# Performance work log

Hardware: AMD Instinct MI355X
Metric: run time of the kernel (lower is better)

## Reference

```python
import jax, jax.numpy as jnp
import numpy as np

T, NI, NK, F, H, O, E = 8, 20000, 50000, 128, 256, 128, 500000


def setup_inputs() -> dict:
    key = jax.random.key(0)
    ks = jax.random.split(key, 32)
    s = 0.05
    inp = {
        "x_inf": jax.random.normal(ks[0], (T, NI, F), jnp.float32),
        "x_item": jax.random.normal(ks[1], (T, NK, F), jnp.float32),
        "e1_src": jax.random.randint(ks[2], (T, E), 0, NI, jnp.int32),
        "e1_dst": jax.random.randint(ks[3], (T, E), 0, NK, jnp.int32),
        "e2_src": jax.random.randint(ks[4], (T, E), 0, NK, jnp.int32),
        "e2_dst": jax.random.randint(ks[5], (T, E), 0, NI, jnp.int32),
        "target_idx": 1234,
        # layer 1, edge type a: influencer -> item (dst = item)
        "W1a_l": s * jax.random.normal(ks[6], (H, F), jnp.float32),
        "b1a_l": jnp.zeros((H,), jnp.float32),
        "W1a_r": s * jax.random.normal(ks[7], (H, F), jnp.float32),
        # layer 1, edge type b: item -> influencer (dst = influencer)
        "W1b_l": s * jax.random.normal(ks[8], (H, F), jnp.float32),
        "b1b_l": jnp.zeros((H,), jnp.float32),
        "W1b_r": s * jax.random.normal(ks[9], (H, F), jnp.float32),
        # layer 2, edge type a (dst = item; output unused by the model head, grads are zero)
        "W2a_l": s * jax.random.normal(ks[10], (O, H), jnp.float32),
        "b2a_l": jnp.zeros((O,), jnp.float32),
        "W2a_r": s * jax.random.normal(ks[11], (O, H), jnp.float32),
        # layer 2, edge type b (dst = influencer)
        "W2b_l": s * jax.random.normal(ks[12], (O, H), jnp.float32),
        "b2b_l": jnp.zeros((O,), jnp.float32),
        "W2b_r": s * jax.random.normal(ks[13], (O, H), jnp.float32),
        # GRU (PyTorch gate order: r, z, n)
        "W_ih": s * jax.random.normal(ks[14], (3 * H, O), jnp.float32),
        "W_hh": s * jax.random.normal(ks[15], (3 * H, H), jnp.float32),
        "b_ih": jnp.zeros((3 * H,), jnp.float32),
        "b_hh": jnp.zeros((3 * H,), jnp.float32),
        # attention + prediction head
        "W_att": s * jax.random.normal(ks[16], (1, H), jnp.float32),
        "b_att": jnp.zeros((1,), jnp.float32),
        "W_p1": s * jax.random.normal(ks[17], (H // 2, H), jnp.float32),
        "b_p1": jnp.zeros((H // 2,), jnp.float32),
        "W_p2": s * jax.random.normal(ks[18], (1, H // 2), jnp.float32),
        "b_p2": jnp.zeros((1,), jnp.float32),
    }
    return inp


def _sage(x_src, x_dst, src, dst, Wl, bl, Wr, n_dst):
    # PyG SAGEConv: lin_l(mean_j x_j) + lin_r(x_i); lin_l has bias, lin_r does not
    msg = x_src[src]                                            # [E, F]
    agg = jax.ops.segment_sum(msg, dst, num_segments=n_dst)     # [n_dst, F]
    cnt = jax.ops.segment_sum(jnp.ones_like(dst, dtype=x_src.dtype), dst, num_segments=n_dst)
    mean = agg / jnp.maximum(cnt, 1.0)[:, None]
    return mean @ Wl.T + bl + x_dst @ Wr.T


def reference(x_inf, x_item, e1_src, e1_dst, e2_src, e2_dst, target_idx,
              W1a_l, b1a_l, W1a_r, W1b_l, b1b_l, W1b_r,
              W2a_l, b2a_l, W2a_r, W2b_l, b2b_l, W2b_r,
              W_ih, W_hh, b_ih, b_hh, W_att, b_att, W_p1, b_p1, W_p2, b_p2):
    def step(carry, xs):
        xi, xk, s1, d1, s2, d2 = xs
        # hetero conv1 (aggr='sum' over edge types; each dst type has one incoming edge type)
        h_item = jax.nn.relu(_sage(xi, xk, s1, d1, W1a_l, b1a_l, W1a_r, NK))
        h_inf = jax.nn.relu(_sage(xk, xi, s2, d2, W1b_l, b1b_l, W1b_r, NI))
        # conv2: only the influencer output feeds the head (item output is dead code)
        o_inf = _sage(h_item, h_inf, s2, d2, W2b_l, b2b_l, W2b_r, NI)
        return carry, o_inf[target_idx]

    _, seq = jax.lax.scan(step, None, (x_inf, x_item, e1_src, e1_dst, e2_src, e2_dst))  # [T, O]

    def gru_step(h, x):
        gi = x @ W_ih.T + b_ih
        gh = h @ W_hh.T + b_hh
        i_r, i_z, i_n = jnp.split(gi, 3)
        h_r, h_z, h_n = jnp.split(gh, 3)
        r = jax.nn.sigmoid(i_r + h_r)
        z = jax.nn.sigmoid(i_z + h_z)
        n = jnp.tanh(i_n + r * h_n)
        h_new = (1.0 - z) * n + z * h
        return h_new, h_new

    h0 = jnp.zeros((H,), seq.dtype)
    _, rnn = jax.lax.scan(gru_step, h0, seq)                    # [T, H]

    att = jax.nn.softmax(rnn @ W_att.T + b_att, axis=0)         # [T, 1]
    ctx = jnp.sum(att * rnn, axis=0)                            # [H]
    hid = jax.nn.relu(ctx @ W_p1.T + b_p1)
    score = (hid @ W_p2.T + b_p2)[0]
    return score
```

## Files before the change

### kernel.cpp

```cpp
#include <hip/hip_runtime.h>
#include <math.h>

#define T 8
#define NI 20000
#define NK 50000
#define F 128
#define H 256
#define O 128
#define E 500000
#define G3 (3*H)
#define MAXS 256
#define CAP1 256
#define BMW 1568
#define NB 8
#define RPB 32
#define EQ (E/4)

#define OFF_CNT2   0
#define OFF_ITEMS  32
#define OFF_CNT1   (32 + T*MAXS*4)
#define OFF_HSUM   (OFF_CNT1 + T*MAXS*4)
#define OFF_BAR    (OFF_HSUM + T*H*4)
#define OFF_GBM    (OFF_BAR + 64)
#define WS_ZERO    (OFF_GBM + T*BMW*4)
#define OFF_LIST1  WS_ZERO
#define OFF_GI     (OFF_LIST1 + (size_t)T*MAXS*CAP1*4)
#define OFF_RNN    (OFF_GI + T*G3*4)
#define WS_USED    (OFF_RNN + T*H*4)

__global__ void k_find_e2(const int* __restrict__ e2_src, const int* __restrict__ e2_dst,
                          const int* __restrict__ target_p,
                          int* __restrict__ cnt2, int* __restrict__ items,
                          unsigned* __restrict__ gbm) {
    int t = blockIdx.y;
    long q = (long)blockIdx.x * 256 + threadIdx.x;
    if (q >= EQ) return;
    int target = *target_p;
    const int4 d4 = ((const int4*)(e2_dst + (long)t * E))[q];
    int dd[4] = {d4.x, d4.y, d4.z, d4.w};
#pragma unroll
    for (int c = 0; c < 4; ++c) {
        if (dd[c] == target) {
            long j = q * 4 + c;
            int src = e2_src[(long)t * E + j];
            int pos = atomicAdd(&cnt2[t], 1);
            if (pos < MAXS) {
                items[t * MAXS + pos] = src;
                atomicOr(&gbm[t * BMW + (src >> 5)], 1u << (src & 31));
            }
        }
    }
}

__global__ void k_scan_e1(const int* __restrict__ e1_src, const int* __restrict__ e1_dst,
                          const int* __restrict__ cnt2, const int* __restrict__ items,
                          const unsigned* __restrict__ gbm,
                          int* __restrict__ cnt1, int* __restrict__ list1) {
    int t = blockIdx.y;
    long q = (long)blockIdx.x * 256 + threadIdx.x;
    if (q >= EQ) return;
    const unsigned* bm = gbm + t * BMW;
    const int4 d4 = ((const int4*)(e1_dst + (long)t * E))[q];
    int dd[4] = {d4.x, d4.y, d4.z, d4.w};
#pragma unroll
    for (int c = 0; c < 4; ++c) {
        int d = dd[c];
        if (!((bm[d >> 5] >> (d & 31)) & 1u)) continue;
        long j = q * 4 + c;
        int src = e1_src[(long)t * E + j];
        int ns = min(cnt2[t], MAXS);
        for (int i = 0; i < ns; ++i) {
            if (items[t * MAXS + i] == d) {
                int pos = atomicAdd(&cnt1[t * MAXS + i], 1);
                if (pos < CAP1) list1[((long)t * MAXS + i) * CAP1 + pos] = src;
            }
        }
    }
}

__global__ void k_hitem(const float* __restrict__ x_item, const float* __restrict__ x_inf,
                        const float* __restrict__ W1a_l, const float* __restrict__ b1a_l,
                        const float* __restrict__ W1a_r,
                        const int* __restrict__ cnt2, const int* __restrict__ items,
                        const int* __restrict__ cnt1, const int* __restrict__ list1,
                        float* __restrict__ hsum) {
    int t = blockIdx.y, slot = blockIdx.x;
    int ns = min(cnt2[t], MAXS);
    if (slot >= ns) return;
    __shared__ float z1[F], xk[F];
    int item = items[t * MAXS + slot];
    int ne = cnt1[t * MAXS + slot];
    float inv = 1.0f / fmaxf((float)ne, 1.0f);
    int nr = min(ne, CAP1);
    if (threadIdx.x < F) {
        int f = threadIdx.x;
        const int* lst = list1 + ((long)t * MAXS + slot) * CAP1;
        float s = 0.0f;
        for (int e = 0; e < nr; ++e)
            s += x_inf[((long)t * NI + lst[e]) * F + f];
        z1[f] = s * inv;
        xk[f] = x_item[((long)t * NK + item) * F + f];
    }
    __syncthreads();
    int h = threadIdx.x;
    float acc = b1a_l[h];
    const float* wl = W1a_l + h * F;
    const float* wr = W1a_r + h * F;
    for (int f = 0; f < F; ++f) acc += z1[f] * wl[f] + xk[f] * wr[f];
    acc = fmaxf(acc, 0.0f);
    atomicAdd(&hsum[t * H + h], acc);
}

__global__ void __launch_bounds__(256, 1)
k_gru(const float* __restrict__ x_inf, const float* __restrict__ x_item,
      const int* __restrict__ target_p,
      const float* __restrict__ W1b_l, const float* __restrict__ b1b_l,
      const float* __restrict__ W1b_r,
      const float* __restrict__ W2b_l, const float* __restrict__ b2b_l,
      const float* __restrict__ W2b_r,
      const int* __restrict__ cnt2, const int* __restrict__ items,
      const float* __restrict__ hsum,
      const float* __restrict__ W_ih, const float* __restrict__ b_ih,
      const float* __restrict__ W_hh, const float* __restrict__ b_hh,
      const float* __restrict__ W_att, const float* __restrict__ b_att,
      const float* __restrict__ W_p1, const float* __restrict__ b_p1,
      const float* __restrict__ W_p2, const float* __restrict__ b_p2,
      float* __restrict__ gi, float* __restrict__ rnn,
      int* __restrict__ bar, float* __restrict__ out) {
    __shared__ float w[3 * RPB][H];
    __shared__ float h[H];
    __shared__ float srnn[T][H];
    __shared__ float satt[T], tmp[H], hid[128];
    __shared__ float z2[F], xt[F], hinf[H], mh[H], so[O];
    int b = blockIdx.x, tid = threadIdx.x;
    int wv = tid >> 6, lane = tid & 63;

    {
        int t = b;
        int target = *target_p;
        int ns = min(cnt2[t], MAXS);
        float c2 = fmaxf((float)cnt2[t], 1.0f);
        if (tid < F) {
            int f = tid;
            float s = 0.0f;
            for (int i = 0; i < ns; ++i)
                s += x_item[((long)t * NK + items[t * MAXS + i]) * F + f];
            z2[f] = s / c2;
            xt[f] = x_inf[((long)t * NI + target) * F + f];
        }
        __syncthreads();
        {
            float acc = b1b_l[tid];
            const float* wl = W1b_l + tid * F;
            const float* wr = W1b_r + tid * F;
            for (int f = 0; f < F; ++f) acc += z2[f] * wl[f] + xt[f] * wr[f];
            hinf[tid] = fmaxf(acc, 0.0f);
            mh[tid] = hsum[t * H + tid] / c2;
        }
        __syncthreads();
        if (tid < O) {
            float acc = b2b_l[tid];
            const float* wl = W2b_l + tid * H;
            const float* wr = W2b_r + tid * H;
            for (int k = 0; k < H; ++k) acc += mh[k] * wl[k] + hinf[k] * wr[k];
            so[tid] = acc;
        }
        __syncthreads();
        for (int row = wv; row < G3; row += 4) {
            const float* wih = W_ih + (long)row * O;
            float s = wih[lane] * so[lane] + wih[lane + 64] * so[lane + 64];
            for (int off = 32; off; off >>= 1) s += __shfl_down(s, off);
            if (lane == 0)
                __hip_atomic_store(&gi[t * G3 + row], s + b_ih[row],
                                   __ATOMIC_RELAXED, __HIP_MEMORY_SCOPE_AGENT);
        }
    }
    __syncthreads();
    if (tid == 0) {
        __threadfence();
        __hip_atomic_fetch_add(&bar[8], 1, __ATOMIC_RELEASE, __HIP_MEMORY_SCOPE_AGENT);
    }
    for (int idx = tid; idx < 3 * RPB * H; idx += 256) {
        int r = idx >> 8, k = idx & 255;
        int g = r / RPB, j = r - g * RPB;
        w[r][k] = W_hh[((long)(g * H + b * RPB + j)) * H + k];
    }
    h[tid] = 0.0f;
    if (tid == 0) {
        while (__hip_atomic_load(&bar[8], __ATOMIC_ACQUIRE, __HIP_MEMORY_SCOPE_AGENT) < NB)
            __builtin_amdgcn_s_sleep(1);
        __threadfence();
    }
    __syncthreads();

    for (int t = 0; t < T; ++t) {
        for (int j = wv; j < RPB; j += 4) {
            float sr = 0.f, sz = 0.f, sn = 0.f;
            for (int c = 0; c < 4; ++c) {
                int k = lane + 64 * c;
                float hk = h[k];
                sr += w[j][k] * hk;
                sz += w[RPB + j][k] * hk;
                sn += w[2 * RPB + j][k] * hk;
            }
            for (int off = 32; off; off >>= 1) {
                sr += __shfl_down(sr, off);
                sz += __shfl_down(sz, off);
                sn += __shfl_down(sn, off);
            }
            if (lane == 0) {
                int i = b * RPB + j;
                float gir = __hip_atomic_load(&gi[t * G3 + i], __ATOMIC_RELAXED,
                                              __HIP_MEMORY_SCOPE_AGENT);
                float giz = __hip_atomic_load(&gi[t * G3 + H + i], __ATOMIC_RELAXED,
                                              __HIP_MEMORY_SCOPE_AGENT);
                float gin = __hip_atomic_load(&gi[t * G3 + 2 * H + i], __ATOMIC_RELAXED,
                                              __HIP_MEMORY_SCOPE_AGENT);
                float r = 1.0f / (1.0f + expf(-(gir + sr + b_hh[i])));
                float z = 1.0f / (1.0f + expf(-(giz + sz + b_hh[H + i])));
                float n = tanhf(gin + r * (sn + b_hh[2 * H + i]));
                float hn = (1.0f - z) * n + z * h[i];
                __hip_atomic_store(&rnn[t * H + i], hn, __ATOMIC_RELAXED,
                                   __HIP_MEMORY_SCOPE_AGENT);
            }
        }
        __syncthreads();
        if (tid == 0) {
            __threadfence();
            __hip_atomic_fetch_add(&bar[t], 1, __ATOMIC_RELEASE, __HIP_MEMORY_SCOPE_AGENT);
            while (__hip_atomic_load(&bar[t], __ATOMIC_ACQUIRE, __HIP_MEMORY_SCOPE_AGENT) < NB)
                __builtin_amdgcn_s_sleep(1);
            __threadfence();
        }
        __syncthreads();
        h[tid] = __hip_atomic_load(&rnn[t * H + tid], __ATOMIC_RELAXED,
                                   __HIP_MEMORY_SCOPE_AGENT);
        __syncthreads();
    }
    if (b != 0) return;
    for (int idx = tid; idx < T * H; idx += 256)
        srnn[idx >> 8][idx & 255] = __hip_atomic_load(&rnn[idx], __ATOMIC_RELAXED,
                                                      __HIP_MEMORY_SCOPE_AGENT);
    __syncthreads();
    {
        int tt = tid >> 5, l32 = tid & 31;
        float a = 0.f;
        for (int c = 0; c < 8; ++c) {
            int k = l32 + 32 * c;
            a += W_att[k] * srnn[tt][k];
        }
        for (int off = 16; off; off >>= 1) a += __shfl_down(a, off, 32);
        if (l32 == 0) satt[tt] = a + b_att[0];
    }
    __syncthreads();
    if (tid == 0) {
        float m = satt[0];
        for (int t = 1; t < T; ++t) m = fmaxf(m, satt[t]);
        float s = 0.f;
        for (int t = 0; t < T; ++t) { satt[t] = expf(satt[t] - m); s += satt[t]; }
        for (int t = 0; t < T; ++t) satt[t] /= s;
    }
    __syncthreads();
    {
        float ctx = 0.f;
        for (int t = 0; t < T; ++t) ctx += satt[t] * srnn[t][tid];
        tmp[tid] = ctx;
    }
    __syncthreads();
    if (tid < 128) {
        float a = b_p1[tid];
        const float* wp = W_p1 + (long)tid * H;
        for (int k = 0; k < H; ++k) a += wp[k] * tmp[k];
        hid[tid] = fmaxf(a, 0.0f);
    }
    __syncthreads();
    if (tid == 0) {
        float s = b_p2[0];
        for (int k = 0; k < 128; ++k) s += W_p2[k] * hid[k];
        out[0] = s;
    }
}

extern "C" void kernel_launch(void* const* d_in, const int* in_sizes, int n_in,
                              void* d_out, int out_size, void* d_ws, size_t ws_size,
                              hipStream_t stream) {
    const float* x_inf  = (const float*)d_in[0];
    const float* x_item = (const float*)d_in[1];
    const int* e1_src = (const int*)d_in[2];
    const int* e1_dst = (const int*)d_in[3];
    const int* e2_src = (const int*)d_in[4];
    const int* e2_dst = (const int*)d_in[5];
    const int* target_p = (const int*)d_in[6];
    const float* W1a_l = (const float*)d_in[7];
    const float* b1a_l = (const float*)d_in[8];
    const float* W1a_r = (const float*)d_in[9];
    const float* W1b_l = (const float*)d_in[10];
    const float* b1b_l = (const float*)d_in[11];
    const float* W1b_r = (const float*)d_in[12];
    const float* W2b_l = (const float*)d_in[16];
    const float* b2b_l = (const float*)d_in[17];
    const float* W2b_r = (const float*)d_in[18];
    const float* W_ih = (const float*)d_in[19];
    const float* W_hh = (const float*)d_in[20];
    const float* b_ih = (const float*)d_in[21];
    const float* b_hh = (const float*)d_in[22];
    const float* W_att = (const float*)d_in[23];
    const float* b_att = (const float*)d_in[24];
    const float* W_p1 = (const float*)d_in[25];
    const float* b_p1 = (const float*)d_in[26];
    const float* W_p2 = (const float*)d_in[27];
    const float* b_p2 = (const float*)d_in[28];
    float* out = (float*)d_out;

    char* ws = (char*)d_ws;
    int*      cnt2  = (int*)(ws + OFF_CNT2);
    int*      items = (int*)(ws + OFF_ITEMS);
    int*      cnt1  = (int*)(ws + OFF_CNT1);
    float*    hsum  = (float*)(ws + OFF_HSUM);
    int*      bar   = (int*)(ws + OFF_BAR);
    unsigned* gbm   = (unsigned*)(ws + OFF_GBM);
    int*      list1 = (int*)(ws + OFF_LIST1);
    float*    gi    = (float*)(ws + OFF_GI);
    float*    rnn   = (float*)(ws + OFF_RNN);

    hipMemsetAsync(d_ws, 0, WS_ZERO, stream);

    dim3 g1((EQ + 255) / 256, T);
    k_find_e2<<<g1, 256, 0, stream>>>(e2_src, e2_dst, target_p, cnt2, items, gbm);

    k_scan_e1<<<g1, 256, 0, stream>>>(e1_src, e1_dst, cnt2, items, gbm, cnt1, list1);

    dim3 g3(MAXS, T);
    k_hitem<<<g3, 256, 0, stream>>>(x_item, x_inf, W1a_l, b1a_l, W1a_r,
                                    cnt2, items, cnt1, list1, hsum);

    k_gru<<<NB, 256, 0, stream>>>(x_inf, x_item, target_p,
                                  W1b_l, b1b_l, W1b_r, W2b_l, b2b_l, W2b_r,
                                  cnt2, items, hsum, W_ih, b_ih, W_hh, b_hh,
                                  W_att, b_att, W_p1, b_p1, W_p2, b_p2,
                                  gi, rnn, bar, out);
}
```

Measured before the change: 699.9 us.

## Split GRU input projection across blocks and coalesce per-step layer matvecs

The per-timestep SAGE matvecs are rewritten so that each wavefront handles one output row with coalesced lane-strided weight loads and a shuffle reduction. This replaces the earlier one-thread-per-row strided loops. The W_ih projection is no longer done by each block for its own timestep over all 768 rows. Instead every block first publishes its layer-2 output, and after a grid barrier each block computes a 96-row slice of W_ih for all eight timesteps, reusing the weights held in registers. The needed gi values are then cached in shared memory, so the recurrent loop stops doing global atomic loads; the cost is one extra grid-wide barrier.

After: 669.3 us. 1.05x faster.

```diff
diff --git a/kernel.cpp b/kernel.cpp
--- a/kernel.cpp
+++ b/kernel.cpp
@@ -14,6 +14,7 @@
 #define BMW 1568
 #define NB 8
 #define RPB 32
+#define GROWS (G3/NB)
 #define EQ (E/4)
 
 #define OFF_CNT2   0
@@ -26,7 +27,8 @@
 #define OFF_LIST1  WS_ZERO
 #define OFF_GI     (OFF_LIST1 + (size_t)T*MAXS*CAP1*4)
 #define OFF_RNN    (OFF_GI + T*G3*4)
-#define WS_USED    (OFF_RNN + T*H*4)
+#define OFF_O      (OFF_RNN + T*H*4)
+#define WS_USED    (OFF_O + T*O*4)
 
 __global__ void k_find_e2(const int* __restrict__ e2_src, const int* __restrict__ e2_dst,
                           const int* __restrict__ target_p,
@@ -125,13 +127,15 @@
       const float* __restrict__ W_att, const float* __restrict__ b_att,
       const float* __restrict__ W_p1, const float* __restrict__ b_p1,
       const float* __restrict__ W_p2, const float* __restrict__ b_p2,
-      float* __restrict__ gi, float* __restrict__ rnn,
+      float* __restrict__ gi, float* __restrict__ rnn, float* __restrict__ o_ws,
       int* __restrict__ bar, float* __restrict__ out) {
     __shared__ float w[3 * RPB][H];
     __shared__ float h[H];
     __shared__ float srnn[T][H];
     __shared__ float satt[T], tmp[H], hid[128];
-    __shared__ float z2[F], xt[F], hinf[H], mh[H], so[O];
+    __shared__ float z2[F], xt[F], hinf[H], mh[H];
+    __shared__ float so_all[T][O];
+    __shared__ float sgi[T][3][RPB];
     int b = blockIdx.x, tid = threadIdx.x;
     int wv = tid >> 6, lane = tid & 63;
 
@@ -148,30 +152,26 @@
             z2[f] = s / c2;
             xt[f] = x_inf[((long)t * NI + target) * F + f];
         }
-        __syncthreads();
-        {
-            float acc = b1b_l[tid];
-            const float* wl = W1b_l + tid * F;
-            const float* wr = W1b_r + tid * F;
-            for (int f = 0; f < F; ++f) acc += z2[f] * wl[f] + xt[f] * wr[f];
-            hinf[tid] = fmaxf(acc, 0.0f);
-            mh[tid] = hsum[t * H + tid] / c2;
-        }
-        __syncthreads();
-        if (tid < O) {
-            float acc = b2b_l[tid];
-            const float* wl = W2b_l + tid * H;
-            const float* wr = W2b_r + tid * H;
-            for (int k = 0; k < H; ++k) acc += mh[k] * wl[k] + hinf[k] * wr[k];
-            so[tid] = acc;
-        }
-        __syncthreads();
-        for (int row = wv; row < G3; row += 4) {
-            const float* wih = W_ih + (long)row * O;
-            float s = wih[lane] * so[lane] + wih[lane + 64] * so[lane + 64];
+        mh[tid] = hsum[t * H + tid] / c2;
+        __syncthreads();
+        for (int r = wv; r < H; r += 4) {
+            float wl0 = W1b_l[r * F + lane],      wl1 = W1b_l[r * F + 64 + lane];
+            float wr0 = W1b_r[r * F + lane],      wr1 = W1b_r[r * F + 64 + lane];
+            float s = wl0 * z2[lane] + wl1 * z2[lane + 64]
+                    + wr0 * xt[lane] + wr1 * xt[lane + 64];
+            for (int off = 32; off; off >>= 1) s += __shfl_down(s, off);
+            if (lane == 0) hinf[r] = fmaxf(s + b1b_l[r], 0.0f);
+        }
+        __syncthreads();
+        for (int r = wv; r < O; r += 4) {
+            float s = 0.0f;
+            for (int c = 0; c < 4; ++c) {
+                int k = lane + 64 * c;
+                s += W2b_l[r * H + k] * mh[k] + W2b_r[r * H + k] * hinf[k];
+            }
             for (int off = 32; off; off >>= 1) s += __shfl_down(s, off);
             if (lane == 0)
-                __hip_atomic_store(&gi[t * G3 + row], s + b_ih[row],
+                __hip_atomic_store(&o_ws[t * O + r], s + b2b_l[r],
                                    __ATOMIC_RELAXED, __HIP_MEMORY_SCOPE_AGENT);
         }
     }
@@ -179,6 +179,33 @@
     if (tid == 0) {
         __threadfence();
         __hip_atomic_fetch_add(&bar[8], 1, __ATOMIC_RELEASE, __HIP_MEMORY_SCOPE_AGENT);
+        while (__hip_atomic_load(&bar[8], __ATOMIC_ACQUIRE, __HIP_MEMORY_SCOPE_AGENT) < NB)
+            __builtin_amdgcn_s_sleep(1);
+        __threadfence();
+    }
+    __syncthreads();
+    for (int idx = tid; idx < T * O; idx += 256)
+        so_all[idx >> 7][idx & 127] = __hip_atomic_load(&o_ws[idx], __ATOMIC_RELAXED,
+                                                        __HIP_MEMORY_SCOPE_AGENT);
+    __syncthreads();
+    for (int lr = wv; lr < GROWS; lr += 4) {
+        int r = b * GROWS + lr;
+        float w0 = W_ih[(long)r * O + lane];
+        float w1 = W_ih[(long)r * O + 64 + lane];
+        float bi = b_ih[r];
+#pragma unroll
+        for (int t = 0; t < T; ++t) {
+            float s = w0 * so_all[t][lane] + w1 * so_all[t][lane + 64];
+            for (int off = 32; off; off >>= 1) s += __shfl_down(s, off);
+            if (lane == 0)
+                __hip_atomic_store(&gi[t * G3 + r], s + bi,
+                                   __ATOMIC_RELAXED, __HIP_MEMORY_SCOPE_AGENT);
+        }
+    }
+    __syncthreads();
+    if (tid == 0) {
+        __threadfence();
+        __hip_atomic_fetch_add(&bar[9], 1, __ATOMIC_RELEASE, __HIP_MEMORY_SCOPE_AGENT);
     }
     for (int idx = tid; idx < 3 * RPB * H; idx += 256) {
         int r = idx >> 8, k = idx & 255;
@@ -187,9 +214,16 @@
     }
     h[tid] = 0.0f;
     if (tid == 0) {
-        while (__hip_atomic_load(&bar[8], __ATOMIC_ACQUIRE, __HIP_MEMORY_SCOPE_AGENT) < NB)
+        while (__hip_atomic_load(&bar[9], __ATOMIC_ACQUIRE, __HIP_MEMORY_SCOPE_AGENT) < NB)
             __builtin_amdgcn_s_sleep(1);
         __threadfence();
+    }
+    __syncthreads();
+    for (int idx = tid; idx < T * 3 * RPB; idx += 256) {
+        int t = idx / 96, rem = idx - t * 96;
+        int g = rem >> 5, j = rem & 31;
+        sgi[t][g][j] = __hip_atomic_load(&gi[t * G3 + g * H + b * RPB + j],
+                                         __ATOMIC_RELAXED, __HIP_MEMORY_SCOPE_AGENT);
     }
     __syncthreads();
 
@@ -210,15 +244,9 @@
             }
             if (lane == 0) {
                 int i = b * RPB + j;
-                float gir = __hip_atomic_load(&gi[t * G3 + i], __ATOMIC_RELAXED,
-                                              __HIP_MEMORY_SCOPE_AGENT);
-                float giz = __hip_atomic_load(&gi[t * G3 + H + i], __ATOMIC_RELAXED,
-                                              __HIP_MEMORY_SCOPE_AGENT);
-                float gin = __hip_atomic_load(&gi[t * G3 + 2 * H + i], __ATOMIC_RELAXED,
-                                              __HIP_MEMORY_SCOPE_AGENT);
-                float r = 1.0f / (1.0f + expf(-(gir + sr + b_hh[i])));
-                float z = 1.0f / (1.0f + expf(-(giz + sz + b_hh[H + i])));
-                float n = tanhf(gin + r * (sn + b_hh[2 * H + i]));
+                float r = 1.0f / (1.0f + expf(-(sgi[t][0][j] + sr + b_hh[i])));
+                float z = 1.0f / (1.0f + expf(-(sgi[t][1][j] + sz + b_hh[H + i])));
+                float n = tanhf(sgi[t][2][j] + r * (sn + b_hh[2 * H + i]));
                 float hn = (1.0f - z) * n + z * h[i];
                 __hip_atomic_store(&rnn[t * H + i], hn, __ATOMIC_RELAXED,
                                    __HIP_MEMORY_SCOPE_AGENT);
@@ -322,6 +350,7 @@
     int*      list1 = (int*)(ws + OFF_LIST1);
     float*    gi    = (float*)(ws + OFF_GI);
     float*    rnn   = (float*)(ws + OFF_RNN);
+    float*    o_ws  = (float*)(ws + OFF_O);
 
     hipMemsetAsync(d_ws, 0, WS_ZERO, stream);
 
@@ -338,5 +367,5 @@
                                   W1b_l, b1b_l, W1b_r, W2b_l, b2b_l, W2b_r,
                                   cnt2, items, hsum, W_ih, b_ih, W_hh, b_hh,
                                   W_att, b_att, W_p1, b_p1, W_p2, b_p2,
-                                  gi, rnn, bar, out);
-}
+                                  gi, rnn, o_ws, bar, out);
+}
```

## Replace GRU grid barriers with sentinel-flag polling and redundant per-block input projection

Applied to the files above, without the earlier changes.

Each GRU block now recomputes the conv-layer and input-projection work for all timesteps itself (only its own W_ih rows), keeping gate inputs in shared memory. That removes the initial cross-block barrier and the global gi buffer. Per-step grid barriers are replaced by polling rnn entries initialised to a 0xFF sentinel by an extra memset, so each thread waits only on the value it needs. This trades redundant compute per block and an extra memset for fewer global synchronisations and atomics.

Result: slower. 808.5 us (+15.5%).

```diff
diff --git a/kernel.cpp b/kernel.cpp
--- a/kernel.cpp
+++ b/kernel.cpp
@@ -15,17 +15,17 @@
 #define NB 8
 #define RPB 32
 #define EQ (E/4)
+#define SENT 0xFFFFFFFFu
 
 #define OFF_CNT2   0
 #define OFF_ITEMS  32
 #define OFF_CNT1   (32 + T*MAXS*4)
 #define OFF_HSUM   (OFF_CNT1 + T*MAXS*4)
-#define OFF_BAR    (OFF_HSUM + T*H*4)
-#define OFF_GBM    (OFF_BAR + 64)
-#define WS_ZERO    (OFF_GBM + T*BMW*4)
-#define OFF_LIST1  WS_ZERO
-#define OFF_GI     (OFF_LIST1 + (size_t)T*MAXS*CAP1*4)
-#define OFF_RNN    (OFF_GI + T*G3*4)
+#define WS_ZERO    (OFF_HSUM + T*H*4)
+#define OFF_GBM    WS_ZERO
+#define WS_ZERO2   (OFF_GBM + T*BMW*4)
+#define OFF_LIST1  WS_ZERO2
+#define OFF_RNN    (OFF_LIST1 + (size_t)T*MAXS*CAP1*4)
 #define WS_USED    (OFF_RNN + T*H*4)
 
 __global__ void k_find_e2(const int* __restrict__ e2_src, const int* __restrict__ e2_dst,
@@ -125,72 +125,83 @@
       const float* __restrict__ W_att, const float* __restrict__ b_att,
       const float* __restrict__ W_p1, const float* __restrict__ b_p1,
       const float* __restrict__ W_p2, const float* __restrict__ b_p2,
-      float* __restrict__ gi, float* __restrict__ rnn,
-      int* __restrict__ bar, float* __restrict__ out) {
+      float* __restrict__ rnn, float* __restrict__ out) {
     __shared__ float w[3 * RPB][H];
     __shared__ float h[H];
     __shared__ float srnn[T][H];
     __shared__ float satt[T], tmp[H], hid[128];
-    __shared__ float z2[F], xt[F], hinf[H], mh[H], so[O];
+    __shared__ float z2a[T][F], xta[T][F];
+    __shared__ float mha[T][H], hinfa[T][H];
+    __shared__ float so_all[T][O];
+    __shared__ float sgi[T][3][RPB];
     int b = blockIdx.x, tid = threadIdx.x;
     int wv = tid >> 6, lane = tid & 63;
-
-    {
-        int t = b;
-        int target = *target_p;
-        int ns = min(cnt2[t], MAXS);
-        float c2 = fmaxf((float)cnt2[t], 1.0f);
-        if (tid < F) {
-            int f = tid;
-            float s = 0.0f;
-            for (int i = 0; i < ns; ++i)
-                s += x_item[((long)t * NK + items[t * MAXS + i]) * F + f];
-            z2[f] = s / c2;
-            xt[f] = x_inf[((long)t * NI + target) * F + f];
-        }
-        __syncthreads();
-        {
-            float acc = b1b_l[tid];
-            const float* wl = W1b_l + tid * F;
-            const float* wr = W1b_r + tid * F;
-            for (int f = 0; f < F; ++f) acc += z2[f] * wl[f] + xt[f] * wr[f];
-            hinf[tid] = fmaxf(acc, 0.0f);
-            mh[tid] = hsum[t * H + tid] / c2;
-        }
-        __syncthreads();
-        if (tid < O) {
-            float acc = b2b_l[tid];
-            const float* wl = W2b_l + tid * H;
-            const float* wr = W2b_r + tid * H;
-            for (int k = 0; k < H; ++k) acc += mh[k] * wl[k] + hinf[k] * wr[k];
-            so[tid] = acc;
-        }
-        __syncthreads();
-        for (int row = wv; row < G3; row += 4) {
-            const float* wih = W_ih + (long)row * O;
-            float s = wih[lane] * so[lane] + wih[lane + 64] * so[lane + 64];
-            for (int off = 32; off; off >>= 1) s += __shfl_down(s, off);
-            if (lane == 0)
-                __hip_atomic_store(&gi[t * G3 + row], s + b_ih[row],
-                                   __ATOMIC_RELAXED, __HIP_MEMORY_SCOPE_AGENT);
-        }
-    }
-    __syncthreads();
-    if (tid == 0) {
-        __threadfence();
-        __hip_atomic_fetch_add(&bar[8], 1, __ATOMIC_RELEASE, __HIP_MEMORY_SCOPE_AGENT);
-    }
+    unsigned* rnn_u = (unsigned*)rnn;
+
     for (int idx = tid; idx < 3 * RPB * H; idx += 256) {
         int r = idx >> 8, k = idx & 255;
         int g = r / RPB, j = r - g * RPB;
         w[r][k] = W_hh[((long)(g * H + b * RPB + j)) * H + k];
     }
+
+    int target = *target_p;
+    for (int p = tid; p < T * F; p += 256) {
+        int t = p >> 7, f = p & 127;
+        int ns = min(cnt2[t], MAXS);
+        float c2 = fmaxf((float)cnt2[t], 1.0f);
+        float s = 0.0f;
+        for (int i = 0; i < ns; ++i)
+            s += x_item[((long)t * NK + items[t * MAXS + i]) * F + f];
+        z2a[t][f] = s / c2;
+        xta[t][f] = x_inf[((long)t * NI + target) * F + f];
+    }
+    for (int p = tid; p < T * H; p += 256) {
+        int t = p >> 8, k = p & 255;
+        float c2 = fmaxf((float)cnt2[t], 1.0f);
+        mha[t][k] = hsum[t * H + k] / c2;
+    }
+    __syncthreads();
+    for (int r = wv; r < H; r += 4) {
+        float wl0 = W1b_l[r * F + lane], wl1 = W1b_l[r * F + 64 + lane];
+        float wr0 = W1b_r[r * F + lane], wr1 = W1b_r[r * F + 64 + lane];
+        float bb = b1b_l[r];
+        for (int t = 0; t < T; ++t) {
+            float s = wl0 * z2a[t][lane] + wl1 * z2a[t][lane + 64]
+                    + wr0 * xta[t][lane] + wr1 * xta[t][lane + 64];
+            for (int off = 32; off; off >>= 1) s += __shfl_down(s, off);
+            if (lane == 0) hinfa[t][r] = fmaxf(s + bb, 0.0f);
+        }
+    }
+    __syncthreads();
+    for (int r = wv; r < O; r += 4) {
+        float a0 = W2b_l[r * H + lane],       a1 = W2b_l[r * H + 64 + lane];
+        float a2 = W2b_l[r * H + 128 + lane], a3 = W2b_l[r * H + 192 + lane];
+        float c0 = W2b_r[r * H + lane],       c1 = W2b_r[r * H + 64 + lane];
+        float c2_ = W2b_r[r * H + 128 + lane], c3 = W2b_r[r * H + 192 + lane];
+        float bb = b2b_l[r];
+        for (int t = 0; t < T; ++t) {
+            float s = a0 * mha[t][lane]       + c0 * hinfa[t][lane]
+                    + a1 * mha[t][lane + 64]  + c1 * hinfa[t][lane + 64]
+                    + a2 * mha[t][lane + 128] + c2_ * hinfa[t][lane + 128]
+                    + a3 * mha[t][lane + 192] + c3 * hinfa[t][lane + 192];
+            for (int off = 32; off; off >>= 1) s += __shfl_down(s, off);
+            if (lane == 0) so_all[t][r] = s + bb;
+        }
+    }
+    __syncthreads();
+    for (int lr = wv; lr < 3 * RPB; lr += 4) {
+        int g = lr >> 5, j = lr & 31;
+        int r = g * H + b * RPB + j;
+        float w0 = W_ih[(long)r * O + lane];
+        float w1 = W_ih[(long)r * O + 64 + lane];
+        float bi = b_ih[r];
+        for (int t = 0; t < T; ++t) {
+            float s = w0 * so_all[t][lane] + w1 * so_all[t][lane + 64];
+            for (int off = 32; off; off >>= 1) s += __shfl_down(s, off);
+            if (lane == 0) sgi[t][g][j] = s + bi;
+        }
+    }
     h[tid] = 0.0f;
-    if (tid == 0) {
-        while (__hip_atomic_load(&bar[8], __ATOMIC_ACQUIRE, __HIP_MEMORY_SCOPE_AGENT) < NB)
-            __builtin_amdgcn_s_sleep(1);
-        __threadfence();
-    }
     __syncthreads();
 
     for (int t = 0; t < T; ++t) {
@@ -210,38 +221,28 @@
             }
             if (lane == 0) {
                 int i = b * RPB + j;
-                float gir = __hip_atomic_load(&gi[t * G3 + i], __ATOMIC_RELAXED,
-                                              __HIP_MEMORY_SCOPE_AGENT);
-                float giz = __hip_atomic_load(&gi[t * G3 + H + i], __ATOMIC_RELAXED,
-                                              __HIP_MEMORY_SCOPE_AGENT);
-                float gin = __hip_atomic_load(&gi[t * G3 + 2 * H + i], __ATOMIC_RELAXED,
-                                              __HIP_MEMORY_SCOPE_AGENT);
-                float r = 1.0f / (1.0f + expf(-(gir + sr + b_hh[i])));
-                float z = 1.0f / (1.0f + expf(-(giz + sz + b_hh[H + i])));
-                float n = tanhf(gin + r * (sn + b_hh[2 * H + i]));
+                float r = 1.0f / (1.0f + expf(-(sgi[t][0][j] + sr + b_hh[i])));
+                float z = 1.0f / (1.0f + expf(-(sgi[t][1][j] + sz + b_hh[H + i])));
+                float n = tanhf(sgi[t][2][j] + r * (sn + b_hh[2 * H + i]));
                 float hn = (1.0f - z) * n + z * h[i];
-                __hip_atomic_store(&rnn[t * H + i], hn, __ATOMIC_RELAXED,
-                                   __HIP_MEMORY_SCOPE_AGENT);
+                __hip_atomic_store(&rnn_u[t * H + i], __float_as_uint(hn),
+                                   __ATOMIC_RELAXED, __HIP_MEMORY_SCOPE_AGENT);
             }
         }
         __syncthreads();
-        if (tid == 0) {
-            __threadfence();
-            __hip_atomic_fetch_add(&bar[t], 1, __ATOMIC_RELEASE, __HIP_MEMORY_SCOPE_AGENT);
-            while (__hip_atomic_load(&bar[t], __ATOMIC_ACQUIRE, __HIP_MEMORY_SCOPE_AGENT) < NB)
-                __builtin_amdgcn_s_sleep(1);
-            __threadfence();
-        }
+        unsigned v;
+        do {
+            v = __hip_atomic_load(&rnn_u[t * H + tid], __ATOMIC_RELAXED,
+                                  __HIP_MEMORY_SCOPE_AGENT);
+            if (v != SENT) break;
+            __builtin_amdgcn_s_sleep(1);
+        } while (true);
+        float hv = __uint_as_float(v);
+        h[tid] = hv;
+        srnn[t][tid] = hv;
         __syncthreads();
-        h[tid] = __hip_atomic_load(&rnn[t * H + tid], __ATOMIC_RELAXED,
-                                   __HIP_MEMORY_SCOPE_AGENT);
-        __syncthreads();
     }
     if (b != 0) return;
-    for (int idx = tid; idx < T * H; idx += 256)
-        srnn[idx >> 8][idx & 255] = __hip_atomic_load(&rnn[idx], __ATOMIC_RELAXED,
-                                                      __HIP_MEMORY_SCOPE_AGENT);
-    __syncthreads();
     {
         int tt = tid >> 5, l32 = tid & 31;
         float a = 0.f;
@@ -317,13 +318,12 @@
     int*      items = (int*)(ws + OFF_ITEMS);
     int*      cnt1  = (int*)(ws + OFF_CNT1);
     float*    hsum  = (float*)(ws + OFF_HSUM);
-    int*      bar   = (int*)(ws + OFF_BAR);
     unsigned* gbm   = (unsigned*)(ws + OFF_GBM);
     int*      list1 = (int*)(ws + OFF_LIST1);
-    float*    gi    = (float*)(ws + OFF_GI);
     float*    rnn   = (float*)(ws + OFF_RNN);
 
-    hipMemsetAsync(d_ws, 0, WS_ZERO, stream);
+    hipMemsetAsync(d_ws, 0, WS_ZERO2, stream);
+    hipMemsetAsync(ws + OFF_RNN, 0xFF, T * H * 4, stream);
 
     dim3 g1((EQ + 255) / 256, T);
     k_find_e2<<<g1, 256, 0, stream>>>(e2_src, e2_dst, target_p, cnt2, items, gbm);
@@ -338,5 +338,5 @@
                                   W1b_l, b1b_l, W1b_r, W2b_l, b2b_l, W2b_r,
                                   cnt2, items, hsum, W_ih, b_ih, W_hh, b_hh,
                                   W_att, b_att, W_p1, b_p1, W_p2, b_p2,
-                                  gi, rnn, bar, out);
-}
+                                  rnn, out);
+}
```
